# Kernel tuning notes

Measured on AMD Instinct MI355X. Metric: run time of the kernel, lower is better.

## Reference

```python
import jax, jax.numpy as jnp
import numpy as np

N, E, F, H, G, C = 50000, 600000, 128, 128, 500, 10
BN_EPS = 1e-5

def setup_inputs() -> dict:
    key = jax.random.key(0)
    ks = jax.random.split(key, 20)
    def lin(k, fan_in, shape):
        b = 1.0 / np.sqrt(fan_in)
        return jax.random.uniform(k, shape, jnp.float32, -b, b)
    inp = {
        'x': jax.random.normal(ks[0], (N, F), jnp.float32),
        'edge_index': jax.random.randint(ks[1], (2, E), 0, N, jnp.int64),
        'batch': jnp.sort(jax.random.randint(ks[2], (N,), 0, G, jnp.int64)),
        # conv1 MLP: Linear(F,H) -> BN(H) -> ReLU -> Dropout -> Linear(H,H) -> ReLU
        'W1a': lin(ks[3], F, (F, H)), 'b1a': lin(ks[4], F, (H,)),
        'g1': jnp.ones((H,), jnp.float32), 'be1': jnp.zeros((H,), jnp.float32),
        'm1': jnp.zeros((H,), jnp.float32), 'v1': jnp.ones((H,), jnp.float32),
        'W1b': lin(ks[5], H, (H, H)), 'b1b': lin(ks[6], H, (H,)),
        # conv2 MLP: Linear(H,H) -> ReLU -> BN(H) -> Dropout -> Linear(H,H) -> ReLU
        'W2a': lin(ks[7], H, (H, H)), 'b2a': lin(ks[8], H, (H,)),
        'g2': jnp.ones((H,), jnp.float32), 'be2': jnp.zeros((H,), jnp.float32),
        'm2': jnp.zeros((H,), jnp.float32), 'v2': jnp.ones((H,), jnp.float32),
        'W2b': lin(ks[9], H, (H, H)), 'b2b': lin(ks[10], H, (H,)),
        # heads
        'Wl1': lin(ks[11], 2 * H, (2 * H, H // 2)), 'bl1': lin(ks[12], 2 * H, (H // 2,)),
        'Wl2': lin(ks[13], H // 2, (H // 2, C)), 'bl2': lin(ks[14], H // 2, (C,)),
    }
    return inp

def _bn(h, g, b, m, v):
    return (h - m) * (g / jnp.sqrt(v + BN_EPS)) + b

def _gin_aggregate(x, src, dst):
    # out[i] = x[i] + sum_{j->i} x[j]  (GINConv with eps=0)
    return x + jax.ops.segment_sum(x[src], dst, num_segments=N)

def reference(x, edge_index, batch,
              W1a, b1a, g1, be1, m1, v1, W1b, b1b,
              W2a, b2a, g2, be2, m2, v2, W2b, b2b,
              Wl1, bl1, Wl2, bl2):
    src, dst = edge_index[0], edge_index[1]
    # conv1
    a1 = _gin_aggregate(x, src, dst)                       # [N, F]
    h1 = _bn(a1 @ W1a + b1a, g1, be1, m1, v1)
    h1 = jax.nn.relu(h1)                                   # dropout = identity (eval)
    h1 = jax.nn.relu(h1 @ W1b + b1b)                       # [N, H]
    # conv2
    a2 = _gin_aggregate(h1, src, dst)                      # [N, H]
    h2 = jax.nn.relu(a2 @ W2a + b2a)
    h2 = _bn(h2, g2, be2, m2, v2)
    h2 = jax.nn.relu(h2 @ W2b + b2b)                       # [N, H]
    # global add pool per graph
    p1 = jax.ops.segment_sum(h1, batch, num_segments=G)    # [G, H]
    p2 = jax.ops.segment_sum(h2, batch, num_segments=G)    # [G, H]
    z = jnp.concatenate((p1, p2), axis=1)                  # [G, 2H]
    z = jax.nn.relu(z @ Wl1 + bl1)
    return z @ Wl2 + bl2                                   # [G, C]
```

## Files before the change

### kernel.cpp

```cpp
#include <hip/hip_runtime.h>

#define N_NODES 50000
#define N_EDGES 600000
#define HDIM 128
#define NGRAPH 500
#define NCLASS 10
#define BN_EPS 1e-5f
#define KSLOT 64
#define KSTRIDE 72

typedef short short8 __attribute__((ext_vector_type(8)));
typedef unsigned short ushort8v __attribute__((ext_vector_type(8)));
typedef float floatx4 __attribute__((ext_vector_type(4)));

__device__ __forceinline__ float bf2f(unsigned short u) {
    unsigned int v = ((unsigned int)u) << 16;
    return __uint_as_float(v);
}
__device__ __forceinline__ unsigned short f2bf(float f) {
    unsigned int u = __float_as_uint(f);
    unsigned int r = (u + 0x7fffu + ((u >> 16) & 1u)) >> 16;
    return (unsigned short)r;
}

__global__ void k_zero(int* __restrict__ cnt) {
    int i = blockIdx.x * blockDim.x + threadIdx.x;
    if (i < N_NODES) cnt[i] = 0;
}

#define ILV 25
#define NB_SCAT 293
#define NB_CAST 6250
#define NB_PREPW 256
#define NB_POOLZ 500
#define NB_SETUP (NB_SCAT * ILV)

__global__ void k_setup(const float* __restrict__ x, unsigned short* __restrict__ xb,
                        const int* __restrict__ src, const int* __restrict__ dst,
                        int* __restrict__ cnt, unsigned short* __restrict__ adj,
                        float* __restrict__ pool,
                        const float* __restrict__ W1a, const float* __restrict__ W1b,
                        const float* __restrict__ W2a, const float* __restrict__ W2b,
                        unsigned short* __restrict__ wpack,
                        const float* __restrict__ b1a, const float* __restrict__ g1,
                        const float* __restrict__ be1, const float* __restrict__ m1,
                        const float* __restrict__ v1, const float* __restrict__ b1b,
                        const float* __restrict__ b2a, const float* __restrict__ g2,
                        const float* __restrict__ be2, const float* __restrict__ m2,
                        const float* __restrict__ v2, const float* __restrict__ b2b,
                        float* __restrict__ ep) {
    int b = blockIdx.x;
    int t = threadIdx.x;
    if (b % ILV == 0) {
        int i8 = (b / ILV) * 256 + t;
        if (i8 < N_EDGES / 8) {
            const int4* s4p = (const int4*)src;
            const int4* d4p = (const int4*)dst;
            int4 sa = s4p[i8 * 2], sb = s4p[i8 * 2 + 1];
            int4 da = d4p[i8 * 2], db = d4p[i8 * 2 + 1];
            int p0 = atomicAdd(&cnt[da.x], 1);
            int p1 = atomicAdd(&cnt[da.y], 1);
            int p2 = atomicAdd(&cnt[da.z], 1);
            int p3 = atomicAdd(&cnt[da.w], 1);
            int p4 = atomicAdd(&cnt[db.x], 1);
            int p5 = atomicAdd(&cnt[db.y], 1);
            int p6 = atomicAdd(&cnt[db.z], 1);
            int p7 = atomicAdd(&cnt[db.w], 1);
            adj[da.x * KSTRIDE + (p0 < KSLOT ? p0 : KSTRIDE - 1)] = (unsigned short)sa.x;
            adj[da.y * KSTRIDE + (p1 < KSLOT ? p1 : KSTRIDE - 1)] = (unsigned short)sa.y;
            adj[da.z * KSTRIDE + (p2 < KSLOT ? p2 : KSTRIDE - 1)] = (unsigned short)sa.z;
            adj[da.w * KSTRIDE + (p3 < KSLOT ? p3 : KSTRIDE - 1)] = (unsigned short)sa.w;
            adj[db.x * KSTRIDE + (p4 < KSLOT ? p4 : KSTRIDE - 1)] = (unsigned short)sb.x;
            adj[db.y * KSTRIDE + (p5 < KSLOT ? p5 : KSTRIDE - 1)] = (unsigned short)sb.y;
            adj[db.z * KSTRIDE + (p6 < KSLOT ? p6 : KSTRIDE - 1)] = (unsigned short)sb.z;
            adj[db.w * KSTRIDE + (p7 < KSLOT ? p7 : KSTRIDE - 1)] = (unsigned short)sb.w;
        }
        return;
    }
    b = b - b / ILV - 1;
    if (b < NB_CAST) {
        int i = b * 256 + t;
        float4 v = ((const float4*)x)[i];
        ushort4 o;
        o.x = f2bf(v.x); o.y = f2bf(v.y); o.z = f2bf(v.z); o.w = f2bf(v.w);
        ((ushort4*)xb)[i] = o;
        return;
    }
    b -= NB_CAST;
    if (b < NB_PREPW) {
        int e = b * 256 + t;
        int w = e >> 14;
        int s_ = e & 16383;
        int j = s_ & 7;
        int m = (s_ >> 3) & 15;
        int q = (s_ >> 7) & 3;
        int ks = (s_ >> 9) & 3;
        int ct = (s_ >> 11) & 7;
        int n = ct * 16 + m;
        int k;
        float scale = 1.f;
        if (w == 0 || w == 2) {
            k = ks * 32 + q * 8 + j;
        } else {
            k = (ks * 2 + (j >> 2)) * 16 + q * 4 + (j & 3);
            if (w == 3) scale = g2[k] * rsqrtf(v2[k] + BN_EPS);
        }
        const float* W = (w == 0) ? W1a : (w == 1) ? W1b : (w == 2) ? W2a : W2b;
        wpack[e] = f2bf(W[k * 128 + n] * scale);
        return;
    }
    b -= NB_PREPW;
    if (b < NB_POOLZ) {
        int i = b * 256 + t;
        pool[i] = 0.f;
        return;
    }
    b -= NB_POOLZ;
    if (b != 0) return;
    if (t < 128) {
        int j = t;
        float s1 = g1[j] * rsqrtf(v1[j] + BN_EPS);
        ep[0 * 256 + 0 + j]   = s1;
        ep[0 * 256 + 128 + j] = (b1a[j] - m1[j]) * s1 + be1[j];
        ep[1 * 256 + 0 + j]   = 1.f;
        ep[1 * 256 + 128 + j] = b2a[j];
        ep[512 + j] = b1b[j];
        float acc = b2b[j];
        for (int k = 0; k < 128; k++) {
            float s2k = g2[k] * rsqrtf(v2[k] + BN_EPS);
            acc += (be2[k] - m2[k] * s2k) * W2b[k * 128 + j];
        }
        ep[512 + 128 + j] = acc;
    }
}

__global__ __launch_bounds__(256) void k_agg(const unsigned short* __restrict__ x,
                                             const int* __restrict__ cnt,
                                             const unsigned short* __restrict__ adj,
                                             unsigned short* __restrict__ out) {
    int g = blockIdx.x * 256 + threadIdx.x;
    int node = g >> 4;
    int m = g & 15;
    if (node >= N_NODES) return;

    int len = cnt[node];
    if (len > KSLOT) len = KSLOT;
    const unsigned short* ad = adj + node * KSTRIDE;

    ushort8v ra = *(const ushort8v*)(ad);

    float self[8];
    {
        short8 sv = *(const short8*)(x + (size_t)node * 128 + m * 8);
        #pragma unroll
        for (int j = 0; j < 8; j++) self[j] = bf2f((unsigned short)sv[j]);
    }
    float acc[8];
    #pragma unroll
    for (int j = 0; j < 8; j++) acc[j] = self[j];

    int nb = (len + 7) >> 3;
    for (int b = 0; b < nb; b++) {
        int i = b * 8;
        ushort8v na = *(const ushort8v*)(ad + i + 8);
        int u0 = (i + 0 < len) ? (int)ra[0] : node;
        int u1 = (i + 1 < len) ? (int)ra[1] : node;
        int u2 = (i + 2 < len) ? (int)ra[2] : node;
        int u3 = (i + 3 < len) ? (int)ra[3] : node;
        int u4 = (i + 4 < len) ? (int)ra[4] : node;
        int u5 = (i + 5 < len) ? (int)ra[5] : node;
        int u6 = (i + 6 < len) ? (int)ra[6] : node;
        int u7 = (i + 7 < len) ? (int)ra[7] : node;
        short8 f0 = *(const short8*)(x + (size_t)u0 * 128 + m * 8);
        short8 f1 = *(const short8*)(x + (size_t)u1 * 128 + m * 8);
        short8 f2 = *(const short8*)(x + (size_t)u2 * 128 + m * 8);
        short8 f3 = *(const short8*)(x + (size_t)u3 * 128 + m * 8);
        short8 f4 = *(const short8*)(x + (size_t)u4 * 128 + m * 8);
        short8 f5 = *(const short8*)(x + (size_t)u5 * 128 + m * 8);
        short8 f6 = *(const short8*)(x + (size_t)u6 * 128 + m * 8);
        short8 f7 = *(const short8*)(x + (size_t)u7 * 128 + m * 8);
        #pragma unroll
        for (int j = 0; j < 8; j++) {
            float a = bf2f((unsigned short)f0[j]) + bf2f((unsigned short)f1[j]) +
                      bf2f((unsigned short)f2[j]) + bf2f((unsigned short)f3[j]);
            float c = bf2f((unsigned short)f4[j]) + bf2f((unsigned short)f5[j]) +
                      bf2f((unsigned short)f6[j]) + bf2f((unsigned short)f7[j]);
            acc[j] += a + c;
        }
        ra = na;
    }
    float extra = (float)(nb * 8 - len);
    #pragma unroll
    for (int j = 0; j < 8; j++) acc[j] -= extra * self[j];

    short8 r;
    #pragma unroll
    for (int j = 0; j < 8; j++) r[j] = (short)f2bf(acc[j]);
    *(short8*)(out + (size_t)node * 128 + m * 8) = r;
}

__global__ __launch_bounds__(256, 2) void k_mlp(const unsigned short* __restrict__ A,
                                                const unsigned short* __restrict__ WaP,
                                                const unsigned short* __restrict__ WbP,
                                                const float* __restrict__ epi,
                                                const float* __restrict__ epf,
                                                const int* __restrict__ batch,
                                                float* __restrict__ poolc,
                                                unsigned short* __restrict__ Out, int n) {
    __shared__ unsigned short Wl[2][16384];
    __shared__ float ps[16][132];
    int t = threadIdx.x;
    int lane = t & 63;
    int w = t >> 6;
    int q = lane >> 4;
    int m = lane & 15;

    int rowbase0 = blockIdx.x * 64;
    int base = rowbase0 + w * 16;
    int node = base + m;
    if (node >= n) node = n - 1;

    short8 a1[4];
    #pragma unroll
    for (int s = 0; s < 4; s++)
        a1[s] = *(const short8*)(A + (size_t)node * 128 + s * 32 + q * 8);

    #pragma unroll
    for (int i = 0; i < 8; i++) {
        int c = t + 256 * i;
        *(short8*)(&Wl[0][c * 8]) = *(const short8*)(WaP + c * 8);
        *(short8*)(&Wl[1][c * 8]) = *(const short8*)(WbP + c * 8);
    }
    __syncthreads();

    int lbase = lane * 8;

    floatx4 acc1[8];
    #pragma unroll
    for (int c = 0; c < 8; c++) acc1[c] = (floatx4)0.f;
    #pragma unroll
    for (int s = 0; s < 4; s++) {
        #pragma unroll
        for (int ct = 0; ct < 8; ct++) {
            short8 wf = *(const short8*)(&Wl[0][(ct * 4 + s) * 512 + lbase]);
            acc1[ct] = __builtin_amdgcn_mfma_f32_16x16x32_bf16(wf, a1[s], acc1[ct], 0, 0, 0);
        }
    }

    short8 a2[4];
    #pragma unroll
    for (int s = 0; s < 4; s++) {
        #pragma unroll
        for (int j = 0; j < 8; j++) {
            int ct = s * 2 + (j >> 2);
            int r = j & 3;
            int col = ct * 16 + q * 4 + r;
            float P = epi[col], Q = epi[128 + col];
            float v = fmaxf(fmaf(acc1[ct][r], P, Q), 0.f);
            a2[s][j] = (short)f2bf(v);
        }
    }

    floatx4 acc2[8];
    #pragma unroll
    for (int c = 0; c < 8; c++) acc2[c] = (floatx4)0.f;
    #pragma unroll
    for (int s = 0; s < 4; s++) {
        #pragma unroll
        for (int ct = 0; ct < 8; ct++) {
            short8 wf = *(const short8*)(&Wl[1][(ct * 4 + s) * 512 + lbase]);
            acc2[ct] = __builtin_amdgcn_mfma_f32_16x16x32_bf16(a2[s], wf, acc2[ct], 0, 0, 0);
        }
    }

    #pragma unroll
    for (int ct = 0; ct < 8; ct++) {
        float Qf = epf[ct * 16 + m];
        #pragma unroll
        for (int r = 0; r < 4; r++) acc2[ct][r] = fmaxf(acc2[ct][r] + Qf, 0.f);
    }

    if (Out) {
        #pragma unroll
        for (int ct = 0; ct < 8; ct++) {
            int col = ct * 16 + m;
            #pragma unroll
            for (int r = 0; r < 4; r++) {
                int gr = base + q * 4 + r;
                if (gr < n)
                    Out[(size_t)gr * 128 + col] = f2bf(acc2[ct][r]);
            }
        }
    }

    int mygid[4];
    #pragma unroll
    for (int r = 0; r < 4; r++) {
        int gr = base + q * 4 + r;
        mygid[r] = (gr < n) ? batch[gr] : -1;
    }
    int lastrow = rowbase0 + 63;
    if (lastrow > n - 1) lastrow = n - 1;
    int g0 = batch[rowbase0];
    int g1 = batch[lastrow];
    for (int g = g0; g <= g1; g++) {
        float pv[8];
        #pragma unroll
        for (int ct = 0; ct < 8; ct++) pv[ct] = 0.f;
        #pragma unroll
        for (int r = 0; r < 4; r++) {
            if (mygid[r] == g) {
                #pragma unroll
                for (int ct = 0; ct < 8; ct++) pv[ct] += acc2[ct][r];
            }
        }
        #pragma unroll
        for (int ct = 0; ct < 8; ct++) ps[w * 4 + q][ct * 16 + m] = pv[ct];
        __syncthreads();
        if (t < 128) {
            float s = 0.f;
            #pragma unroll
            for (int k = 0; k < 16; k++) s += ps[k][t];
            atomicAdd(&poolc[g * 256 + t], s);
        }
        __syncthreads();
    }
}

__global__ void k_head(const float* __restrict__ pool, const float* __restrict__ Wl1,
                       const float* __restrict__ bl1, const float* __restrict__ Wl2,
                       const float* __restrict__ bl2, float* __restrict__ out) {
    int g = blockIdx.x;
    int t = threadIdx.x;
    __shared__ float zmid[64];
    const float* z = pool + g * 256;
    float acc = bl1[t];
    #pragma unroll 8
    for (int k = 0; k < 256; k++) acc = fmaf(z[k], Wl1[k * 64 + t], acc);
    zmid[t] = fmaxf(acc, 0.f);
    __syncthreads();
    if (t < NCLASS) {
        float a = bl2[t];
        #pragma unroll
        for (int j = 0; j < 64; j++) a = fmaf(zmid[j], Wl2[j * 10 + t], a);
        out[g * NCLASS + t] = a;
    }
}


extern "C" void kernel_launch(void* const* d_in, const int* in_sizes, int n_in,
                              void* d_out, int out_size, void* d_ws, size_t ws_size,
                              hipStream_t stream) {
    const float* x   = (const float*)d_in[0];
    const int* eidx  = (const int*)d_in[1];
    const int* batch = (const int*)d_in[2];
    const float* W1a = (const float*)d_in[3];
    const float* b1a = (const float*)d_in[4];
    const float* g1  = (const float*)d_in[5];
    const float* be1 = (const float*)d_in[6];
    const float* m1  = (const float*)d_in[7];
    const float* v1  = (const float*)d_in[8];
    const float* W1b = (const float*)d_in[9];
    const float* b1b = (const float*)d_in[10];
    const float* W2a = (const float*)d_in[11];
    const float* b2a = (const float*)d_in[12];
    const float* g2  = (const float*)d_in[13];
    const float* be2 = (const float*)d_in[14];
    const float* m2  = (const float*)d_in[15];
    const float* v2  = (const float*)d_in[16];
    const float* W2b = (const float*)d_in[17];
    const float* b2b = (const float*)d_in[18];
    const float* Wl1 = (const float*)d_in[19];
    const float* bl1 = (const float*)d_in[20];
    const float* Wl2 = (const float*)d_in[21];
    const float* bl2 = (const float*)d_in[22];
    const int* srcv = eidx;
    const int* dstv = eidx + N_EDGES;

    char* ws = (char*)d_ws;
    size_t off = 0;
    auto alloc = [&](size_t bytes) -> void* {
        void* p = ws + off;
        off = (off + bytes + 255) & ~(size_t)255;
        return p;
    };
    int* cnt      = (int*)alloc(sizeof(int) * N_NODES);
    unsigned short* adj = (unsigned short*)alloc(sizeof(unsigned short) * (size_t)N_NODES * KSTRIDE);
    float* ep     = (float*)alloc(sizeof(float) * 768);
    float* pool   = (float*)alloc(sizeof(float) * NGRAPH * 256);
    unsigned short* wpack = (unsigned short*)alloc(sizeof(unsigned short) * 4 * 16384);
    unsigned short* xb    = (unsigned short*)alloc(sizeof(unsigned short) * (size_t)N_NODES * HDIM);
    unsigned short* bufA  = (unsigned short*)alloc(sizeof(unsigned short) * (size_t)N_NODES * HDIM);
    unsigned short* bufC  = (unsigned short*)alloc(sizeof(unsigned short) * (size_t)N_NODES * HDIM);
    (void)ws_size; (void)in_sizes; (void)n_in; (void)out_size;

    float* outp = (float*)d_out;

    k_zero<<<dim3((N_NODES + 255) / 256), dim3(256), 0, stream>>>(cnt);
    k_setup<<<dim3(NB_SETUP), dim3(256), 0, stream>>>(
        x, xb, srcv, dstv, cnt, adj, pool, W1a, W1b, W2a, W2b, wpack,
        b1a, g1, be1, m1, v1, b1b, b2a, g2, be2, m2, v2, b2b, ep);

    dim3 agrid((N_NODES * 16 + 255) / 256), ablk(256);
    dim3 mgrid((N_NODES + 63) / 64), mblk(256);

    k_agg<<<agrid, ablk, 0, stream>>>(xb, cnt, adj, bufA);
    k_mlp<<<mgrid, mblk, 0, stream>>>(bufA, wpack + 0 * 16384, wpack + 1 * 16384,
                                      ep + 0, ep + 512, batch, pool + 0, bufC, N_NODES);
    k_agg<<<agrid, ablk, 0, stream>>>(bufC, cnt, adj, bufA);
    k_mlp<<<mgrid, mblk, 0, stream>>>(bufA, wpack + 2 * 16384, wpack + 3 * 16384,
                                      ep + 256, ep + 640, batch, pool + 128, nullptr, N_NODES);
    k_head<<<dim3(NGRAPH), dim3(64), 0, stream>>>(pool, Wl1, bl1, Wl2, bl2, outp);
}
```

Baseline: 224.9 us.

## Fuse neighbor aggregation with MLP per 16-node tile and replace pooling atomics

```diff
diff --git a/kernel.cpp b/kernel.cpp
--- a/kernel.cpp
+++ b/kernel.cpp
@@ -8,6 +8,7 @@
 #define BN_EPS 1e-5f
 #define KSLOT 64
 #define KSTRIDE 72
+#define NBLK 3125
 
 typedef short short8 __attribute__((ext_vector_type(8)));
 typedef unsigned short ushort8v __attribute__((ext_vector_type(8)));
@@ -28,17 +29,17 @@
     if (i < N_NODES) cnt[i] = 0;
 }
 
-#define ILV 25
+#define ILV 24
 #define NB_SCAT 293
 #define NB_CAST 6250
 #define NB_PREPW 256
-#define NB_POOLZ 500
+#define NB_OFF 197
 #define NB_SETUP (NB_SCAT * ILV)
 
 __global__ void k_setup(const float* __restrict__ x, unsigned short* __restrict__ xb,
                         const int* __restrict__ src, const int* __restrict__ dst,
                         int* __restrict__ cnt, unsigned short* __restrict__ adj,
-                        float* __restrict__ pool,
+                        const int* __restrict__ batch, int* __restrict__ off,
                         const float* __restrict__ W1a, const float* __restrict__ W1b,
                         const float* __restrict__ W2a, const float* __restrict__ W2b,
                         unsigned short* __restrict__ wpack,
@@ -97,25 +98,23 @@
         int ks = (s_ >> 9) & 3;
         int ct = (s_ >> 11) & 7;
         int n = ct * 16 + m;
-        int k;
-        float scale = 1.f;
-        if (w == 0 || w == 2) {
-            k = ks * 32 + q * 8 + j;
-        } else {
-            k = (ks * 2 + (j >> 2)) * 16 + q * 4 + (j & 3);
-            if (w == 3) scale = g2[k] * rsqrtf(v2[k] + BN_EPS);
-        }
+        int k = ks * 32 + q * 8 + j;
+        float scale = (w == 3) ? g2[k] * rsqrtf(v2[k] + BN_EPS) : 1.f;
         const float* W = (w == 0) ? W1a : (w == 1) ? W1b : (w == 2) ? W2a : W2b;
         wpack[e] = f2bf(W[k * 128 + n] * scale);
         return;
     }
     b -= NB_PREPW;
-    if (b < NB_POOLZ) {
+    if (b < NB_OFF) {
         int i = b * 256 + t;
-        pool[i] = 0.f;
+        if (i <= N_NODES) {
+            int glo = (i == 0) ? 0 : batch[i - 1] + 1;
+            int ghi = (i == N_NODES) ? NGRAPH : batch[i];
+            for (int g = glo; g <= ghi; g++) off[g] = i;
+        }
         return;
     }
-    b -= NB_POOLZ;
+    b -= NB_OFF;
     if (b != 0) return;
     if (t < 128) {
         int j = t;
@@ -134,215 +133,228 @@
     }
 }
 
-__global__ __launch_bounds__(256) void k_agg(const unsigned short* __restrict__ x,
-                                             const int* __restrict__ cnt,
-                                             const unsigned short* __restrict__ adj,
-                                             unsigned short* __restrict__ out) {
-    int g = blockIdx.x * 256 + threadIdx.x;
-    int node = g >> 4;
-    int m = g & 15;
-    if (node >= N_NODES) return;
-
-    int len = cnt[node];
-    if (len > KSLOT) len = KSLOT;
-    const unsigned short* ad = adj + node * KSTRIDE;
-
-    ushort8v ra = *(const ushort8v*)(ad);
-
-    float self[8];
+__global__ __launch_bounds__(256, 4) void k_conv(const unsigned short* __restrict__ X,
+                                                 const int* __restrict__ cnt,
+                                                 const unsigned short* __restrict__ adj,
+                                                 const unsigned short* __restrict__ WaP,
+                                                 const unsigned short* __restrict__ WbP,
+                                                 const float* __restrict__ epi,
+                                                 const float* __restrict__ epf,
+                                                 const int* __restrict__ batch,
+                                                 float* __restrict__ partial,
+                                                 int* __restrict__ pgid,
+                                                 unsigned short* __restrict__ Out) {
+    __shared__ unsigned short Wl[16384];
+    __shared__ unsigned short htile[2048];
+    __shared__ float ps[2][4][128];
+    int t = threadIdx.x;
+    int base = blockIdx.x * 16;
+
+    #pragma unroll
+    for (int i = 0; i < 8; i++) {
+        int c = t + 256 * i;
+        *(short8*)(&Wl[c * 8]) = *(const short8*)(WaP + c * 8);
+    }
+
     {
-        short8 sv = *(const short8*)(x + (size_t)node * 128 + m * 8);
-        #pragma unroll
-        for (int j = 0; j < 8; j++) self[j] = bf2f((unsigned short)sv[j]);
-    }
-    float acc[8];
-    #pragma unroll
-    for (int j = 0; j < 8; j++) acc[j] = self[j];
-
-    int nb = (len + 7) >> 3;
-    for (int b = 0; b < nb; b++) {
-        int i = b * 8;
-        ushort8v na = *(const ushort8v*)(ad + i + 8);
-        int u0 = (i + 0 < len) ? (int)ra[0] : node;
-        int u1 = (i + 1 < len) ? (int)ra[1] : node;
-        int u2 = (i + 2 < len) ? (int)ra[2] : node;
-        int u3 = (i + 3 < len) ? (int)ra[3] : node;
-        int u4 = (i + 4 < len) ? (int)ra[4] : node;
-        int u5 = (i + 5 < len) ? (int)ra[5] : node;
-        int u6 = (i + 6 < len) ? (int)ra[6] : node;
-        int u7 = (i + 7 < len) ? (int)ra[7] : node;
-        short8 f0 = *(const short8*)(x + (size_t)u0 * 128 + m * 8);
-        short8 f1 = *(const short8*)(x + (size_t)u1 * 128 + m * 8);
-        short8 f2 = *(const short8*)(x + (size_t)u2 * 128 + m * 8);
-        short8 f3 = *(const short8*)(x + (size_t)u3 * 128 + m * 8);
-        short8 f4 = *(const short8*)(x + (size_t)u4 * 128 + m * 8);
-        short8 f5 = *(const short8*)(x + (size_t)u5 * 128 + m * 8);
-        short8 f6 = *(const short8*)(x + (size_t)u6 * 128 + m * 8);
-        short8 f7 = *(const short8*)(x + (size_t)u7 * 128 + m * 8);
-        #pragma unroll
-        for (int j = 0; j < 8; j++) {
-            float a = bf2f((unsigned short)f0[j]) + bf2f((unsigned short)f1[j]) +
-                      bf2f((unsigned short)f2[j]) + bf2f((unsigned short)f3[j]);
-            float c = bf2f((unsigned short)f4[j]) + bf2f((unsigned short)f5[j]) +
-                      bf2f((unsigned short)f6[j]) + bf2f((unsigned short)f7[j]);
-            acc[j] += a + c;
-        }
-        ra = na;
-    }
-    float extra = (float)(nb * 8 - len);
-    #pragma unroll
-    for (int j = 0; j < 8; j++) acc[j] -= extra * self[j];
-
-    short8 r;
-    #pragma unroll
-    for (int j = 0; j < 8; j++) r[j] = (short)f2bf(acc[j]);
-    *(short8*)(out + (size_t)node * 128 + m * 8) = r;
-}
-
-__global__ __launch_bounds__(256, 2) void k_mlp(const unsigned short* __restrict__ A,
-                                                const unsigned short* __restrict__ WaP,
-                                                const unsigned short* __restrict__ WbP,
-                                                const float* __restrict__ epi,
-                                                const float* __restrict__ epf,
-                                                const int* __restrict__ batch,
-                                                float* __restrict__ poolc,
-                                                unsigned short* __restrict__ Out, int n) {
-    __shared__ unsigned short Wl[2][16384];
-    __shared__ float ps[16][132];
-    int t = threadIdx.x;
+        int node_l = t >> 4;
+        int m = t & 15;
+        int node = base + node_l;
+        int len = cnt[node];
+        if (len > KSLOT) len = KSLOT;
+        const unsigned short* ad = adj + node * KSTRIDE;
+        ushort8v ra = *(const ushort8v*)(ad);
+        float self[8];
+        {
+            short8 sv = *(const short8*)(X + (size_t)node * 128 + m * 8);
+            #pragma unroll
+            for (int j = 0; j < 8; j++) self[j] = bf2f((unsigned short)sv[j]);
+        }
+        float acc[8];
+        #pragma unroll
+        for (int j = 0; j < 8; j++) acc[j] = self[j];
+        int nb = (len + 7) >> 3;
+        for (int bb = 0; bb < nb; bb++) {
+            int i = bb * 8;
+            ushort8v na = *(const ushort8v*)(ad + i + 8);
+            int u0 = (i + 0 < len) ? (int)ra[0] : node;
+            int u1 = (i + 1 < len) ? (int)ra[1] : node;
+            int u2 = (i + 2 < len) ? (int)ra[2] : node;
+            int u3 = (i + 3 < len) ? (int)ra[3] : node;
+            int u4 = (i + 4 < len) ? (int)ra[4] : node;
+            int u5 = (i + 5 < len) ? (int)ra[5] : node;
+            int u6 = (i + 6 < len) ? (int)ra[6] : node;
+            int u7 = (i + 7 < len) ? (int)ra[7] : node;
+            short8 f0 = *(const short8*)(X + (size_t)u0 * 128 + m * 8);
+            short8 f1 = *(const short8*)(X + (size_t)u1 * 128 + m * 8);
+            short8 f2 = *(const short8*)(X + (size_t)u2 * 128 + m * 8);
+            short8 f3 = *(const short8*)(X + (size_t)u3 * 128 + m * 8);
+            short8 f4 = *(const short8*)(X + (size_t)u4 * 128 + m * 8);
+            short8 f5 = *(const short8*)(X + (size_t)u5 * 128 + m * 8);
+            short8 f6 = *(const short8*)(X + (size_t)u6 * 128 + m * 8);
+            short8 f7 = *(const short8*)(X + (size_t)u7 * 128 + m * 8);
+            #pragma unroll
+            for (int j = 0; j < 8; j++) {
+                float a = bf2f((unsigned short)f0[j]) + bf2f((unsigned short)f1[j]) +
+                          bf2f((unsigned short)f2[j]) + bf2f((unsigned short)f3[j]);
+                float c = bf2f((unsigned short)f4[j]) + bf2f((unsigned short)f5[j]) +
+                          bf2f((unsigned short)f6[j]) + bf2f((unsigned short)f7[j]);
+                acc[j] += a + c;
+            }
+            ra = na;
+        }
+        float extra = (float)(nb * 8 - len);
+        short8 hv;
+        #pragma unroll
+        for (int j = 0; j < 8; j++) hv[j] = (short)f2bf(acc[j] - extra * self[j]);
+        int hb = node_l * 256 + ((m * 16) ^ ((node_l & 7) << 4));
+        *(short8*)((char*)htile + hb) = hv;
+    }
+    __syncthreads();
+
     int lane = t & 63;
     int w = t >> 6;
     int q = lane >> 4;
-    int m = lane & 15;
-
-    int rowbase0 = blockIdx.x * 64;
-    int base = rowbase0 + w * 16;
-    int node = base + m;
-    if (node >= n) node = n - 1;
-
-    short8 a1[4];
+    int mm = lane & 15;
+    int lbase = lane * 8;
+
+    short8 a[4];
     #pragma unroll
     for (int s = 0; s < 4; s++)
-        a1[s] = *(const short8*)(A + (size_t)node * 128 + s * 32 + q * 8);
-
+        a[s] = *(const short8*)((char*)htile + mm * 256 + ((s * 64 + q * 16) ^ ((mm & 7) << 4)));
+
+    floatx4 acc1[2];
+    acc1[0] = (floatx4)0.f; acc1[1] = (floatx4)0.f;
+    #pragma unroll
+    for (int c = 0; c < 2; c++) {
+        int ct = w * 2 + c;
+        #pragma unroll
+        for (int s = 0; s < 4; s++) {
+            short8 wf = *(const short8*)(&Wl[(ct * 4 + s) * 512 + lbase]);
+            acc1[c] = __builtin_amdgcn_mfma_f32_16x16x32_bf16(a[s], wf, acc1[c], 0, 0, 0);
+        }
+    }
+    __syncthreads();
+
+    #pragma unroll
+    for (int c = 0; c < 2; c++) {
+        int ct = w * 2 + c;
+        int col = ct * 16 + mm;
+        float P = epi[col], Q = epi[128 + col];
+        #pragma unroll
+        for (int r = 0; r < 4; r++) {
+            int row = q * 4 + r;
+            float v = fmaxf(fmaf(acc1[c][r], P, Q), 0.f);
+            int byte = row * 256 + (((unsigned)(col * 2)) ^ ((row & 7) << 4));
+            *(unsigned short*)((char*)htile + byte) = f2bf(v);
+        }
+    }
     #pragma unroll
     for (int i = 0; i < 8; i++) {
         int c = t + 256 * i;
-        *(short8*)(&Wl[0][c * 8]) = *(const short8*)(WaP + c * 8);
-        *(short8*)(&Wl[1][c * 8]) = *(const short8*)(WbP + c * 8);
-    }
-    __syncthreads();
-
-    int lbase = lane * 8;
-
-    floatx4 acc1[8];
-    #pragma unroll
-    for (int c = 0; c < 8; c++) acc1[c] = (floatx4)0.f;
-    #pragma unroll
-    for (int s = 0; s < 4; s++) {
-        #pragma unroll
-        for (int ct = 0; ct < 8; ct++) {
-            short8 wf = *(const short8*)(&Wl[0][(ct * 4 + s) * 512 + lbase]);
-            acc1[ct] = __builtin_amdgcn_mfma_f32_16x16x32_bf16(wf, a1[s], acc1[ct], 0, 0, 0);
-        }
-    }
-
-    short8 a2[4];
-    #pragma unroll
-    for (int s = 0; s < 4; s++) {
-        #pragma unroll
-        for (int j = 0; j < 8; j++) {
-            int ct = s * 2 + (j >> 2);
-            int r = j & 3;
-            int col = ct * 16 + q * 4 + r;
-            float P = epi[col], Q = epi[128 + col];
-            float v = fmaxf(fmaf(acc1[ct][r], P, Q), 0.f);
-            a2[s][j] = (short)f2bf(v);
-        }
-    }
-
-    floatx4 acc2[8];
-    #pragma unroll
-    for (int c = 0; c < 8; c++) acc2[c] = (floatx4)0.f;
-    #pragma unroll
-    for (int s = 0; s < 4; s++) {
-        #pragma unroll
-        for (int ct = 0; ct < 8; ct++) {
-            short8 wf = *(const short8*)(&Wl[1][(ct * 4 + s) * 512 + lbase]);
-            acc2[ct] = __builtin_amdgcn_mfma_f32_16x16x32_bf16(a2[s], wf, acc2[ct], 0, 0, 0);
-        }
-    }
-
-    #pragma unroll
-    for (int ct = 0; ct < 8; ct++) {
-        float Qf = epf[ct * 16 + m];
-        #pragma unroll
-        for (int r = 0; r < 4; r++) acc2[ct][r] = fmaxf(acc2[ct][r] + Qf, 0.f);
+        *(short8*)(&Wl[c * 8]) = *(const short8*)(WbP + c * 8);
+    }
+    __syncthreads();
+
+    #pragma unroll
+    for (int s = 0; s < 4; s++)
+        a[s] = *(const short8*)((char*)htile + mm * 256 + ((s * 64 + q * 16) ^ ((mm & 7) << 4)));
+
+    floatx4 acc2[2];
+    acc2[0] = (floatx4)0.f; acc2[1] = (floatx4)0.f;
+    #pragma unroll
+    for (int c = 0; c < 2; c++) {
+        int ct = w * 2 + c;
+        #pragma unroll
+        for (int s = 0; s < 4; s++) {
+            short8 wf = *(const short8*)(&Wl[(ct * 4 + s) * 512 + lbase]);
+            acc2[c] = __builtin_amdgcn_mfma_f32_16x16x32_bf16(a[s], wf, acc2[c], 0, 0, 0);
+        }
+    }
+
+    #pragma unroll
+    for (int c = 0; c < 2; c++) {
+        int col = (w * 2 + c) * 16 + mm;
+        float Qf = epf[col];
+        #pragma unroll
+        for (int r = 0; r < 4; r++) acc2[c][r] = fmaxf(acc2[c][r] + Qf, 0.f);
     }
 
     if (Out) {
         #pragma unroll
-        for (int ct = 0; ct < 8; ct++) {
-            int col = ct * 16 + m;
+        for (int c = 0; c < 2; c++) {
+            int col = (w * 2 + c) * 16 + mm;
             #pragma unroll
-            for (int r = 0; r < 4; r++) {
-                int gr = base + q * 4 + r;
-                if (gr < n)
-                    Out[(size_t)gr * 128 + col] = f2bf(acc2[ct][r]);
-            }
-        }
-    }
-
+            for (int r = 0; r < 4; r++)
+                Out[(size_t)(base + q * 4 + r) * 128 + col] = f2bf(acc2[c][r]);
+        }
+    }
+
+    int g0 = batch[base];
+    int g1b = batch[base + 15];
+    int gs1 = (g1b != g0) ? g1b : -1;
     int mygid[4];
     #pragma unroll
-    for (int r = 0; r < 4; r++) {
-        int gr = base + q * 4 + r;
-        mygid[r] = (gr < n) ? batch[gr] : -1;
-    }
-    int lastrow = rowbase0 + 63;
-    if (lastrow > n - 1) lastrow = n - 1;
-    int g0 = batch[rowbase0];
-    int g1 = batch[lastrow];
-    for (int g = g0; g <= g1; g++) {
-        float pv[8];
-        #pragma unroll
-        for (int ct = 0; ct < 8; ct++) pv[ct] = 0.f;
-        #pragma unroll
-        for (int r = 0; r < 4; r++) {
-            if (mygid[r] == g) {
-                #pragma unroll
-                for (int ct = 0; ct < 8; ct++) pv[ct] += acc2[ct][r];
-            }
-        }
-        #pragma unroll
-        for (int ct = 0; ct < 8; ct++) ps[w * 4 + q][ct * 16 + m] = pv[ct];
-        __syncthreads();
-        if (t < 128) {
-            float s = 0.f;
+    for (int r = 0; r < 4; r++) mygid[r] = batch[base + q * 4 + r];
+    #pragma unroll
+    for (int k = 0; k < 2; k++) {
+        int gk = k ? gs1 : g0;
+        #pragma unroll
+        for (int c = 0; c < 2; c++) {
+            float pv = 0.f;
             #pragma unroll
-            for (int k = 0; k < 16; k++) s += ps[k][t];
-            atomicAdd(&poolc[g * 256 + t], s);
-        }
-        __syncthreads();
-    }
-}
-
-__global__ void k_head(const float* __restrict__ pool, const float* __restrict__ Wl1,
-                       const float* __restrict__ bl1, const float* __restrict__ Wl2,
-                       const float* __restrict__ bl2, float* __restrict__ out) {
+            for (int r = 0; r < 4; r++)
+                if (mygid[r] == gk) pv += acc2[c][r];
+            ps[k][q][(w * 2 + c) * 16 + mm] = pv;
+        }
+    }
+    __syncthreads();
+    {
+        int kk = t >> 7, col = t & 127;
+        float s = ps[kk][0][col] + ps[kk][1][col] + ps[kk][2][col] + ps[kk][3][col];
+        partial[((size_t)blockIdx.x * 2 + kk) * 128 + col] = s;
+        if (t == 0) pgid[blockIdx.x * 2] = g0;
+        if (t == 1) pgid[blockIdx.x * 2 + 1] = gs1;
+    }
+}
+
+__global__ void k_head(const int* __restrict__ off, const int* __restrict__ pgid,
+                       const float* __restrict__ partial1, const float* __restrict__ partial2,
+                       const float* __restrict__ Wl1, const float* __restrict__ bl1,
+                       const float* __restrict__ Wl2, const float* __restrict__ bl2,
+                       float* __restrict__ out) {
     int g = blockIdx.x;
     int t = threadIdx.x;
-    __shared__ float zmid[64];
-    const float* z = pool + g * 256;
-    float acc = bl1[t];
-    #pragma unroll 8
-    for (int k = 0; k < 256; k++) acc = fmaf(z[k], Wl1[k * 64 + t], acc);
-    zmid[t] = fmaxf(acc, 0.f);
+    __shared__ float zL[256];
+    __shared__ float zm[64];
+    float z1 = 0.f, z2 = 0.f;
+    int r0 = off[g], r1 = off[g + 1];
+    if (r1 > r0) {
+        int b0 = r0 >> 4, b1 = (r1 - 1) >> 4;
+        for (int b = b0; b <= b1; b++) {
+            #pragma unroll
+            for (int k = 0; k < 2; k++) {
+                if (pgid[b * 2 + k] == g) {
+                    z1 += partial1[((size_t)b * 2 + k) * 128 + t];
+                    z2 += partial2[((size_t)b * 2 + k) * 128 + t];
+                }
+            }
+        }
+    }
+    zL[t] = z1;
+    zL[128 + t] = z2;
+    __syncthreads();
+    if (t < 64) {
+        float acc = bl1[t];
+        #pragma unroll 8
+        for (int k = 0; k < 256; k++) acc = fmaf(zL[k], Wl1[k * 64 + t], acc);
+        zm[t] = fmaxf(acc, 0.f);
+    }
     __syncthreads();
     if (t < NCLASS) {
         float a = bl2[t];
         #pragma unroll
-        for (int j = 0; j < 64; j++) a = fmaf(zmid[j], Wl2[j * 10 + t], a);
+        for (int j = 0; j < 64; j++) a = fmaf(zm[j], Wl2[j * 10 + t], a);
         out[g * NCLASS + t] = a;
     }
 }
@@ -378,37 +390,37 @@
     const int* dstv = eidx + N_EDGES;
 
     char* ws = (char*)d_ws;
-    size_t off = 0;
+    size_t offb = 0;
     auto alloc = [&](size_t bytes) -> void* {
-        void* p = ws + off;
-        off = (off + bytes + 255) & ~(size_t)255;
+        void* p = ws + offb;
+        offb = (offb + bytes + 255) & ~(size_t)255;
         return p;
     };
     int* cnt      = (int*)alloc(sizeof(int) * N_NODES);
     unsigned short* adj = (unsigned short*)alloc(sizeof(unsigned short) * (size_t)N_NODES * KSTRIDE);
     float* ep     = (float*)alloc(sizeof(float) * 768);
-    float* pool   = (float*)alloc(sizeof(float) * NGRAPH * 256);
     unsigned short* wpack = (unsigned short*)alloc(sizeof(unsigned short) * 4 * 16384);
     unsigned short* xb    = (unsigned short*)alloc(sizeof(unsigned short) * (size_t)N_NODES * HDIM);
-    unsigned short* bufA  = (unsigned short*)alloc(sizeof(unsigned short) * (size_t)N_NODES * HDIM);
     unsigned short* bufC  = (unsigned short*)alloc(sizeof(unsigned short) * (size_t)N_NODES * HDIM);
+    float* partial1 = (float*)alloc(sizeof(float) * (size_t)NBLK * 2 * 128);
+    float* partial2 = (float*)alloc(sizeof(float) * (size_t)NBLK * 2 * 128);
+    int* pgid     = (int*)alloc(sizeof(int) * NBLK * 2);
+    int* goff     = (int*)alloc(sizeof(int) * (NGRAPH + 1));
     (void)ws_size; (void)in_sizes; (void)n_in; (void)out_size;
 
     float* outp = (float*)d_out;
 
     k_zero<<<dim3((N_NODES + 255) / 256), dim3(256), 0, stream>>>(cnt);
     k_setup<<<dim3(NB_SETUP), dim3(256), 0, stream>>>(
-        x, xb, srcv, dstv, cnt, adj, pool, W1a, W1b, W2a, W2b, wpack,
+        x, xb, srcv, dstv, cnt, adj, batch, goff, W1a, W1b, W2a, W2b, wpack,
         b1a, g1, be1, m1, v1, b1b, b2a, g2, be2, m2, v2, b2b, ep);
 
-    dim3 agrid((N_NODES * 16 + 255) / 256), ablk(256);
-    dim3 mgrid((N_NODES + 63) / 64), mblk(256);
-
-    k_agg<<<agrid, ablk, 0, stream>>>(xb, cnt, adj, bufA);
-    k_mlp<<<mgrid, mblk, 0, stream>>>(bufA, wpack + 0 * 16384, wpack + 1 * 16384,
-                                      ep + 0, ep + 512, batch, pool + 0, bufC, N_NODES);
-    k_agg<<<agrid, ablk, 0, stream>>>(bufC, cnt, adj, bufA);
-    k_mlp<<<mgrid, mblk, 0, stream>>>(bufA, wpack + 2 * 16384, wpack + 3 * 16384,
-                                      ep + 256, ep + 640, batch, pool + 128, nullptr, N_NODES);
-    k_head<<<dim3(NGRAPH), dim3(64), 0, stream>>>(pool, Wl1, bl1, Wl2, bl2, outp);
-}
+    k_conv<<<dim3(NBLK), dim3(256), 0, stream>>>(
+        xb, cnt, adj, wpack + 0 * 16384, wpack + 1 * 16384,
+        ep + 0, ep + 512, batch, partial1, pgid, bufC);
+    k_conv<<<dim3(NBLK), dim3(256), 0, stream>>>(
+        bufC, cnt, adj, wpack + 2 * 16384, wpack + 3 * 16384,
+        ep + 256, ep + 640, batch, partial2, pgid, nullptr);
+    k_head<<<dim3(NGRAPH), dim3(128), 0, stream>>>(
+        goff, pgid, partial1, partial2, Wl1, bl1, Wl2, bl2, outp);
+}
```

Result: slower. 263.7 us (+17.2%).

## Split node features into four 32-column planes to shrink aggregation gather footprint

Applied to the files above, without the earlier changes.

```diff
diff --git a/kernel.cpp b/kernel.cpp
--- a/kernel.cpp
+++ b/kernel.cpp
@@ -8,6 +8,7 @@
 #define BN_EPS 1e-5f
 #define KSLOT 64
 #define KSTRIDE 72
+#define SUBSZ ((size_t)N_NODES * 32)
 
 typedef short short8 __attribute__((ext_vector_type(8)));
 typedef unsigned short ushort8v __attribute__((ext_vector_type(8)));
@@ -83,7 +84,9 @@
         float4 v = ((const float4*)x)[i];
         ushort4 o;
         o.x = f2bf(v.x); o.y = f2bf(v.y); o.z = f2bf(v.z); o.w = f2bf(v.w);
-        ((ushort4*)xb)[i] = o;
+        int n = i >> 5;
+        int f4 = i & 31;
+        *(ushort4*)(xb + (size_t)(f4 >> 3) * SUBSZ + (size_t)n * 32 + (f4 & 7) * 4) = o;
         return;
     }
     b -= NB_CAST;
@@ -134,24 +137,29 @@
     }
 }
 
-__global__ __launch_bounds__(256) void k_agg(const unsigned short* __restrict__ x,
+__global__ __launch_bounds__(256) void k_agg(const unsigned short* __restrict__ X,
                                              const int* __restrict__ cnt,
                                              const unsigned short* __restrict__ adj,
                                              unsigned short* __restrict__ out) {
-    int g = blockIdx.x * 256 + threadIdx.x;
-    int node = g >> 4;
-    int m = g & 15;
+    int b = blockIdx.x;
+    int fg = (b & 7) >> 1;
+    int r = ((b >> 3) << 1) | (b & 1);
+    int t = threadIdx.x;
+    int node_l = t >> 2;
+    int m = t & 3;
+    int node = r * 64 + node_l;
     if (node >= N_NODES) return;
 
+    const unsigned short* Xs = X + (size_t)fg * SUBSZ;
     int len = cnt[node];
     if (len > KSLOT) len = KSLOT;
     const unsigned short* ad = adj + node * KSTRIDE;
 
-    ushort8v ra = *(const ushort8v*)(ad);
+    ushort8v ra = __builtin_nontemporal_load((const ushort8v*)ad);
 
     float self[8];
     {
-        short8 sv = *(const short8*)(x + (size_t)node * 128 + m * 8);
+        short8 sv = *(const short8*)(Xs + (size_t)node * 32 + m * 8);
         #pragma unroll
         for (int j = 0; j < 8; j++) self[j] = bf2f((unsigned short)sv[j]);
     }
@@ -160,9 +168,9 @@
     for (int j = 0; j < 8; j++) acc[j] = self[j];
 
     int nb = (len + 7) >> 3;
-    for (int b = 0; b < nb; b++) {
-        int i = b * 8;
-        ushort8v na = *(const ushort8v*)(ad + i + 8);
+    for (int bb = 0; bb < nb; bb++) {
+        int i = bb * 8;
+        ushort8v na = __builtin_nontemporal_load((const ushort8v*)(ad + i + 8));
         int u0 = (i + 0 < len) ? (int)ra[0] : node;
         int u1 = (i + 1 < len) ? (int)ra[1] : node;
         int u2 = (i + 2 < len) ? (int)ra[2] : node;
@@ -171,14 +179,14 @@
         int u5 = (i + 5 < len) ? (int)ra[5] : node;
         int u6 = (i + 6 < len) ? (int)ra[6] : node;
         int u7 = (i + 7 < len) ? (int)ra[7] : node;
-        short8 f0 = *(const short8*)(x + (size_t)u0 * 128 + m * 8);
-        short8 f1 = *(const short8*)(x + (size_t)u1 * 128 + m * 8);
-        short8 f2 = *(const short8*)(x + (size_t)u2 * 128 + m * 8);
-        short8 f3 = *(const short8*)(x + (size_t)u3 * 128 + m * 8);
-        short8 f4 = *(const short8*)(x + (size_t)u4 * 128 + m * 8);
-        short8 f5 = *(const short8*)(x + (size_t)u5 * 128 + m * 8);
-        short8 f6 = *(const short8*)(x + (size_t)u6 * 128 + m * 8);
-        short8 f7 = *(const short8*)(x + (size_t)u7 * 128 + m * 8);
+        short8 f0 = *(const short8*)(Xs + (size_t)u0 * 32 + m * 8);
+        short8 f1 = *(const short8*)(Xs + (size_t)u1 * 32 + m * 8);
+        short8 f2 = *(const short8*)(Xs + (size_t)u2 * 32 + m * 8);
+        short8 f3 = *(const short8*)(Xs + (size_t)u3 * 32 + m * 8);
+        short8 f4 = *(const short8*)(Xs + (size_t)u4 * 32 + m * 8);
+        short8 f5 = *(const short8*)(Xs + (size_t)u5 * 32 + m * 8);
+        short8 f6 = *(const short8*)(Xs + (size_t)u6 * 32 + m * 8);
+        short8 f7 = *(const short8*)(Xs + (size_t)u7 * 32 + m * 8);
         #pragma unroll
         for (int j = 0; j < 8; j++) {
             float a = bf2f((unsigned short)f0[j]) + bf2f((unsigned short)f1[j]) +
@@ -190,13 +198,10 @@
         ra = na;
     }
     float extra = (float)(nb * 8 - len);
-    #pragma unroll
-    for (int j = 0; j < 8; j++) acc[j] -= extra * self[j];
-
-    short8 r;
-    #pragma unroll
-    for (int j = 0; j < 8; j++) r[j] = (short)f2bf(acc[j]);
-    *(short8*)(out + (size_t)node * 128 + m * 8) = r;
+    short8 rv;
+    #pragma unroll
+    for (int j = 0; j < 8; j++) rv[j] = (short)f2bf(acc[j] - extra * self[j]);
+    __builtin_nontemporal_store(rv, (short8*)(out + (size_t)fg * SUBSZ + (size_t)node * 32 + m * 8));
 }
 
 __global__ __launch_bounds__(256, 2) void k_mlp(const unsigned short* __restrict__ A,
@@ -223,7 +228,7 @@
     short8 a1[4];
     #pragma unroll
     for (int s = 0; s < 4; s++)
-        a1[s] = *(const short8*)(A + (size_t)node * 128 + s * 32 + q * 8);
+        a1[s] = *(const short8*)(A + (size_t)s * SUBSZ + (size_t)node * 32 + q * 8);
 
     #pragma unroll
     for (int i = 0; i < 8; i++) {
@@ -284,11 +289,12 @@
         #pragma unroll
         for (int ct = 0; ct < 8; ct++) {
             int col = ct * 16 + m;
+            unsigned short* Os = Out + (size_t)(col >> 5) * SUBSZ + (col & 31);
             #pragma unroll
             for (int r = 0; r < 4; r++) {
                 int gr = base + q * 4 + r;
                 if (gr < n)
-                    Out[(size_t)gr * 128 + col] = f2bf(acc2[ct][r]);
+                    Os[(size_t)gr * 32] = f2bf(acc2[ct][r]);
             }
         }
     }
@@ -378,10 +384,10 @@
     const int* dstv = eidx + N_EDGES;
 
     char* ws = (char*)d_ws;
-    size_t off = 0;
+    size_t offb = 0;
     auto alloc = [&](size_t bytes) -> void* {
-        void* p = ws + off;
-        off = (off + bytes + 255) & ~(size_t)255;
+        void* p = ws + offb;
+        offb = (offb + bytes + 255) & ~(size_t)255;
         return p;
     };
     int* cnt      = (int*)alloc(sizeof(int) * N_NODES);
@@ -401,7 +407,7 @@
         x, xb, srcv, dstv, cnt, adj, pool, W1a, W1b, W2a, W2b, wpack,
         b1a, g1, be1, m1, v1, b1b, b2a, g2, be2, m2, v2, b2b, ep);
 
-    dim3 agrid((N_NODES * 16 + 255) / 256), ablk(256);
+    dim3 agrid(782 * 4), ablk(256);
     dim3 mgrid((N_NODES + 63) / 64), mblk(256);
 
     k_agg<<<agrid, ablk, 0, stream>>>(xb, cnt, adj, bufA);
```

After: 244.8 us. 1.09x slower.
